# Performance work log

Hardware: AMD Instinct MI355X
Metric: run time of the kernel (lower is better)

The kernel has to match this reference:

```python
import jax, jax.numpy as jnp
import numpy as np

B, C, T = 64, 128, 4096
KNOT = 4  # default knot=4 -> 6 spline knots
SIGMA = 0.2


def setup_inputs() -> dict:
    key = jax.random.key(0)
    k1, k2, k3 = jax.random.split(key, 3)
    x = jax.random.normal(k1, (B, C, T), dtype=jnp.float32)
    # yy ~ N(1.0, sigma) as in GenerateRandomCurves
    yy = 1.0 + SIGMA * jax.random.normal(k2, (B, KNOT + 2, C), dtype=jnp.float32)
    mask_rand = jax.random.uniform(k3, (B, 1, 1), dtype=jnp.float32)
    return {"x": x, "yy": yy, "mask_rand": mask_rand}


def _notaknot_matrix(n, h):
    # Moment (second-derivative) system for a not-a-knot cubic spline on a
    # uniform grid with spacing h (matches scipy.interpolate.CubicSpline default bc).
    A = np.zeros((n, n), dtype=np.float32)
    for i in range(1, n - 1):
        A[i, i - 1] = h / 6.0
        A[i, i] = 2.0 * h / 3.0
        A[i, i + 1] = h / 6.0
    # not-a-knot: third derivative continuous at x1 and x_{n-2}
    A[0, 0], A[0, 1], A[0, 2] = 1.0, -2.0, 1.0
    A[-1, -3], A[-1, -2], A[-1, -1] = 1.0, -2.0, 1.0
    return jnp.asarray(A)


def reference(x, yy, mask_rand):
    Bq, Cq, Tq = x.shape
    n = KNOT + 2
    h = (Tq - 1) / (KNOT + 1)  # uniform knot spacing; knots span [0, T-1]
    A = _notaknot_matrix(n, h)

    # Solve for spline moments M (second derivatives at knots), batched over (B, C).
    rhs_int = (yy[:, 2:, :] - 2.0 * yy[:, 1:-1, :] + yy[:, :-2, :]) / h  # (B, n-2, C)
    z = jnp.zeros((Bq, 1, Cq), yy.dtype)
    rhs = jnp.concatenate([z, rhs_int, z], axis=1)  # (B, n, C)
    M = jnp.linalg.solve(A, rhs)  # (B, n, C)

    # Evaluate the spline at t = 0..T-1 (vectorized over all batch/channel).
    tq = jnp.arange(Tq, dtype=x.dtype)
    idx = jnp.clip(jnp.floor(tq / h).astype(jnp.int32), 0, n - 2)  # (T,)
    xl = idx.astype(x.dtype) * h
    dxl = (tq - xl)[None, :, None]       # t - x_i
    dxr = (xl + h - tq)[None, :, None]   # x_{i+1} - t
    Mi, Mi1 = M[:, idx, :], M[:, idx + 1, :]      # (B, T, C)
    yi, yi1 = yy[:, idx, :], yy[:, idx + 1, :]    # (B, T, C)
    curve = ((Mi * dxr**3 + Mi1 * dxl**3) / (6.0 * h)
             + (yi / h - Mi * h / 6.0) * dxr
             + (yi1 / h - Mi1 * h / 6.0) * dxl)   # (B, T, C)

    # DistortTimesteps: cumulative sum, rescaled so the last step lands on T-1.
    tt = jnp.cumsum(curve, axis=1)
    tt = tt * (Tq - 1) / tt[:, -1:, :]  # (B, T, C)

    # Per-(batch, channel) linear interpolation back onto the regular grid.
    xp = tt.transpose(0, 2, 1).reshape(Bq * Cq, Tq)  # warped timestamps
    fp = x.reshape(Bq * Cq, Tq)                      # channel signals
    x_tw = jax.vmap(lambda a, b: jnp.interp(tq, a, b))(xp, fp)
    x_tw = x_tw.reshape(Bq, Cq, Tq)

    mask = mask_rand < 0.5  # (B,1,1): apply warp with probability p=0.5
    return jnp.where(mask, x_tw, x)
```

## Files before the change

kernel.cpp:

```cpp
#include <hip/hip_runtime.h>

#define BB 64
#define CC 128
#define TT 4096
#define NN 6
#define HH 819.0f
#define NTHR 256
#define EPT 16
#define NWAVE (NTHR / 64)
#define NROW (BB * CC)
#define NSPAN 5
#define TABBYTES ((size_t)NROW * NSPAN * 16)
#define PADSZ (TT + TT / 32)

typedef float f4 __attribute__((ext_vector_type(4)));

__device__ __forceinline__ void nt_store4(float* p, f4 v) {
    __builtin_nontemporal_store(v, (f4*)p);
}

__device__ __forceinline__ int padi(int j) { return j + (j >> 5); }

__device__ __forceinline__ void spline_solve(const float* __restrict__ yy,
                                             int b, int c, float* y, float* Mv)
{
    #pragma unroll
    for (int k = 0; k < NN; ++k)
        y[k] = yy[((size_t)b * NN + k) * CC + c];
    float Aug[NN][NN + 1];
    #pragma unroll
    for (int i = 0; i < NN; ++i)
        #pragma unroll
        for (int j = 0; j < NN + 1; ++j)
            Aug[i][j] = 0.0f;
    Aug[0][0] = 1.0f;  Aug[0][1] = -2.0f;  Aug[0][2] = 1.0f;
    Aug[5][3] = 1.0f;  Aug[5][4] = -2.0f;  Aug[5][5] = 1.0f;
    #pragma unroll
    for (int i = 1; i < NN - 1; ++i) {
        Aug[i][i - 1] = HH / 6.0f;
        Aug[i][i]     = 2.0f * HH / 3.0f;
        Aug[i][i + 1] = HH / 6.0f;
        Aug[i][NN]    = (y[i + 1] - 2.0f * y[i] + y[i - 1]) / HH;
    }
    #pragma unroll
    for (int k = 0; k < NN; ++k) {
        float inv = 1.0f / Aug[k][k];
        #pragma unroll
        for (int i = k + 1; i < NN; ++i) {
            float m = Aug[i][k] * inv;
            #pragma unroll
            for (int j = k; j < NN + 1; ++j)
                Aug[i][j] -= m * Aug[k][j];
        }
    }
    #pragma unroll
    for (int i = NN - 1; i >= 0; --i) {
        float s = Aug[i][NN];
        #pragma unroll
        for (int j = i + 1; j < NN; ++j)
            s -= Aug[i][j] * Mv[j];
        Mv[i] = s / Aug[i][i];
    }
}

__device__ __forceinline__ void horner_coefs(const float* y, const float* Mv,
                                             f4* out5)
{
    const float invh  = 1.0f / HH;
    const float inv6h = 1.0f / (6.0f * HH);
    #pragma unroll
    for (int s = 0; s < NSPAN; ++s) {
        f4 cf;
        cf.x = y[s];
        cf.y = (y[s + 1] - y[s]) * invh - Mv[s] * (HH / 3.0f) - Mv[s + 1] * (HH / 6.0f);
        cf.z = Mv[s] * 0.5f;
        cf.w = (Mv[s + 1] - Mv[s]) * inv6h;
        out5[s] = cf;
    }
}

__global__ __launch_bounds__(256) void spline_coef_kernel(
    const float* __restrict__ yy, f4* __restrict__ tab)
{
    const int row = blockIdx.x * 256 + threadIdx.x;
    const int b = row / CC;
    const int c = row % CC;
    float y[NN], Mv[NN];
    spline_solve(yy, b, c, y, Mv);
    f4 cf[NSPAN];
    horner_coefs(y, Mv, cf);
    #pragma unroll
    for (int s = 0; s < NSPAN; ++s)
        tab[row * NSPAN + s] = cf[s];
}

template <int TABLE>
__global__ __launch_bounds__(NTHR, 6) void timewarp_kernel(
    const float* __restrict__ x,
    const float* __restrict__ yy,
    const float* __restrict__ mask_rand,
    const f4* __restrict__ tab,
    float* __restrict__ out)
{
    const int row = blockIdx.x;
    const int b   = row / CC;
    const int tid = threadIdx.x;

    const float* xrow = x + (size_t)row * TT;
    float* orow       = out + (size_t)row * TT;

    if (!(mask_rand[b] < 0.5f)) {
        const f4* xi = (const f4*)xrow;
        #pragma unroll
        for (int k = 0; k < 4; ++k)
            nt_store4(orow + 4 * (tid + NTHR * k), xi[tid + NTHR * k]);
        return;
    }

    __shared__ float sh_res[PADSZ];
    __shared__ float sh_wsum[NWAVE];

    const int t0 = tid * EPT;
    int idxA = t0 / 819;  if (idxA > 4) idxA = 4;
    int idxB = idxA + 1;  if (idxB > 4) idxB = 4;
    const float xlA = (float)idxA * HH;
    const float xlB = (float)idxB * HH;
    const float tb  = (float)((idxA + 1) * 819);

    float fpv[EPT];
    {
        #pragma unroll
        for (int q = 0; q < 4; ++q) {
            const f4 v = *(const f4*)(xrow + t0 + 4 * q);
            fpv[4 * q + 0] = v.x; fpv[4 * q + 1] = v.y;
            fpv[4 * q + 2] = v.z; fpv[4 * q + 3] = v.w;
        }
    }
    const float fpb = xrow[(t0 + EPT < TT) ? (t0 + EPT) : (TT - 1)];

    f4 cfA, cfB;
    if (TABLE) {
        cfA = tab[row * NSPAN + idxA];
        cfB = tab[row * NSPAN + idxB];
    } else {
        float y[NN], Mv[NN];
        f4 cf[NSPAN];
        spline_solve(yy, b, row % CC, y, Mv);
        horner_coefs(y, Mv, cf);
        cfA = cf[0];  cfB = cf[0];
        #pragma unroll
        for (int s = 1; s < NSPAN; ++s) {
            if (idxA >= s) cfA = cf[s];
            if (idxB >= s) cfB = cf[s];
        }
    }

    float xp[EPT + 1];
    float running = 0.0f;
    #pragma unroll
    for (int k = 0; k < EPT; ++k) {
        float ft = (float)(t0 + k);
        bool inB = ft >= tb;
        f4    cf = inB ? cfB : cfA;
        float xl = inB ? xlB : xlA;
        float s  = ft - xl;
        running += fmaf(s, fmaf(s, fmaf(s, cf.w, cf.z), cf.y), cf.x);
        xp[k] = running;
    }
    float cN;
    {
        float ft = (float)(t0 + EPT);
        bool inB = ft >= tb;
        f4    cf = inB ? cfB : cfA;
        float xl = inB ? xlB : xlA;
        float s  = ft - xl;
        cN = fmaf(s, fmaf(s, fmaf(s, cf.w, cf.z), cf.y), cf.x);
    }

    const int lane = tid & 63, wid = tid >> 6;
    float ws = running;
    #pragma unroll
    for (int d = 1; d < 64; d <<= 1) {
        float v = __shfl_up(ws, d, 64);
        if (lane >= d) ws += v;
    }
    if (lane == 63) sh_wsum[wid] = ws;
    __syncthreads();
    float wo = 0.0f, total = 0.0f;
    #pragma unroll
    for (int w = 0; w < NWAVE; ++w) {
        float s = sh_wsum[w];
        total += s;
        if (w < wid) wo += s;
    }
    const float offs  = wo + (ws - running);
    const float scale = 4095.0f / total;

    #pragma unroll
    for (int k = 0; k < EPT; ++k)
        xp[k] = (xp[k] + offs) * scale;

    {
        float n = __shfl_down(xp[0], 1, 64);
        float l = ((wo + ws) + cN) * scale;
        xp[EPT] = (lane == 63) ? l : n;
    }

    #pragma unroll
    for (int k = 0; k < EPT; ++k) {
        const int seg = t0 + k;
        if (seg < TT - 1) {
            float xa = xp[k], xb = xp[k + 1];
            float fa = fpv[k];
            float fb = (k < EPT - 1) ? fpv[k + 1] : fpb;
            float d  = xb - xa;
            float slope = (d > 0.0f) ? (fb - fa) * __builtin_amdgcn_rcpf(d) : 0.0f;
            float a0 = fmaf(-xa, slope, fa);
            int qlo = (int)ceilf(xa);  if (qlo < 0) qlo = 0;
            int qhi = (int)ceilf(xb);  if (qhi > TT) qhi = TT;
            for (int q = qlo; q < qhi; ++q)
                sh_res[padi(q)] = fmaf((float)q, slope, a0);
        }
    }
    if (tid == 0) {
        int q1 = (int)ceilf(xp[0]);  if (q1 > TT) q1 = TT;
        for (int q = 0; q < q1; ++q) sh_res[padi(q)] = fpv[0];
    }
    if (tid == NTHR - 1) {
        int q0 = (int)ceilf(xp[EPT - 1]);  if (q0 < 0) q0 = 0;
        for (int q = q0; q < TT; ++q) sh_res[padi(q)] = fpv[EPT - 1];
    }
    __syncthreads();

    #pragma unroll
    for (int kk = 0; kk < 4; ++kk) {
        int i4  = tid + NTHR * kk;
        int fb4 = 4 * i4;
        int p   = padi(fb4);
        f4 v;
        v.x = sh_res[p + 0];
        v.y = sh_res[p + 1];
        v.z = sh_res[p + 2];
        v.w = sh_res[p + 3];
        nt_store4(orow + fb4, v);
    }
}

extern "C" void kernel_launch(void* const* d_in, const int* in_sizes, int n_in,
                              void* d_out, int out_size, void* d_ws, size_t ws_size,
                              hipStream_t stream) {
    const float* x    = (const float*)d_in[0];
    const float* yy   = (const float*)d_in[1];
    const float* mask = (const float*)d_in[2];
    float* out = (float*)d_out;

    if (d_ws != nullptr && ws_size >= TABBYTES) {
        f4* tab = (f4*)d_ws;
        spline_coef_kernel<<<dim3(NROW / 256), dim3(256), 0, stream>>>(yy, tab);
        timewarp_kernel<1><<<dim3(NROW), dim3(NTHR), 0, stream>>>(x, yy, mask, tab, out);
    } else {
        timewarp_kernel<0><<<dim3(NROW), dim3(NTHR), 0, stream>>>(x, yy, mask, nullptr, out);
    }
}
```

Measured before the change: 241.6 us.

## Replace scatter interpolation with seeded per-quad search over shared xp/fp pairs

Instead of each source segment scattering interpolated values into a shared result buffer, the kernel now stores (xp, fp) pairs in shared memory and writes a coarse seed index for every group of four output positions. Each thread then starts from its seed and walks forward to find the bracketing segment for its four outputs before interpolating. The goal is to cut the per-output scatter work and load imbalance from uneven warping. In exchange it doubles the shared footprint with float2 entries, adds data-dependent while loops, and lowers the launch-bounds occupancy hint from 6 to 4.

```diff
diff --git a/kernel.cpp b/kernel.cpp
--- a/kernel.cpp
+++ b/kernel.cpp
@@ -11,7 +11,8 @@
 #define NROW (BB * CC)
 #define NSPAN 5
 #define TABBYTES ((size_t)NROW * NSPAN * 16)
-#define PADSZ (TT + TT / 32)
+#define NSEED 1024
+#define XFSZ 4224
 
 typedef float f4 __attribute__((ext_vector_type(4)));
 
@@ -19,7 +20,7 @@
     __builtin_nontemporal_store(v, (f4*)p);
 }
 
-__device__ __forceinline__ int padi(int j) { return j + (j >> 5); }
+__device__ __forceinline__ int p2(int j) { return j + (j >> 5); }
 
 __device__ __forceinline__ void spline_solve(const float* __restrict__ yy,
                                              int b, int c, float* y, float* Mv)
@@ -95,7 +96,7 @@
 }
 
 template <int TABLE>
-__global__ __launch_bounds__(NTHR, 6) void timewarp_kernel(
+__global__ __launch_bounds__(NTHR, 4) void timewarp_kernel(
     const float* __restrict__ x,
     const float* __restrict__ yy,
     const float* __restrict__ mask_rand,
@@ -117,8 +118,9 @@
         return;
     }
 
-    __shared__ float sh_res[PADSZ];
-    __shared__ float sh_wsum[NWAVE];
+    __shared__ float2 sh_xf[XFSZ];
+    __shared__ short  sh_seed[NSEED];
+    __shared__ float  sh_wsum[NWAVE];
 
     const int t0 = tid * EPT;
     int idxA = t0 / 819;  if (idxA > 4) idxA = 4;
@@ -136,7 +138,6 @@
             fpv[4 * q + 2] = v.z; fpv[4 * q + 3] = v.w;
         }
     }
-    const float fpb = xrow[(t0 + EPT < TT) ? (t0 + EPT) : (TT - 1)];
 
     f4 cfA, cfB;
     if (TABLE) {
@@ -207,42 +208,59 @@
     }
 
     #pragma unroll
+    for (int k = 0; k < EPT; ++k)
+        sh_xf[p2(t0 + k)] = make_float2(xp[k], fpv[k]);
+
+    #pragma unroll
     for (int k = 0; k < EPT; ++k) {
         const int seg = t0 + k;
         if (seg < TT - 1) {
             float xa = xp[k], xb = xp[k + 1];
-            float fa = fpv[k];
-            float fb = (k < EPT - 1) ? fpv[k + 1] : fpb;
-            float d  = xb - xa;
-            float slope = (d > 0.0f) ? (fb - fa) * __builtin_amdgcn_rcpf(d) : 0.0f;
-            float a0 = fmaf(-xa, slope, fa);
-            int qlo = (int)ceilf(xa);  if (qlo < 0) qlo = 0;
-            int qhi = (int)ceilf(xb);  if (qhi > TT) qhi = TT;
-            for (int q = qlo; q < qhi; ++q)
-                sh_res[padi(q)] = fmaf((float)q, slope, a0);
+            int m = (int)ceilf(xa * 0.25f);  if (m < 0) m = 0;
+            for (; m < NSEED && 4.0f * (float)m < xb; ++m)
+                sh_seed[m] = (short)seg;
         }
     }
     if (tid == 0) {
-        int q1 = (int)ceilf(xp[0]);  if (q1 > TT) q1 = TT;
-        for (int q = 0; q < q1; ++q) sh_res[padi(q)] = fpv[0];
+        int mh = (int)ceilf(xp[0] * 0.25f);  if (mh > NSEED) mh = NSEED;
+        for (int m = 0; m < mh; ++m) sh_seed[m] = (short)-1;
     }
     if (tid == NTHR - 1) {
-        int q0 = (int)ceilf(xp[EPT - 1]);  if (q0 < 0) q0 = 0;
-        for (int q = q0; q < TT; ++q) sh_res[padi(q)] = fpv[EPT - 1];
+        int mt = (int)ceilf(xp[EPT - 1] * 0.25f);  if (mt < 0) mt = 0;
+        for (int m = mt; m < NSEED; ++m) sh_seed[m] = (short)(TT - 1);
     }
     __syncthreads();
 
     #pragma unroll
-    for (int kk = 0; kk < 4; ++kk) {
-        int i4  = tid + NTHR * kk;
-        int fb4 = 4 * i4;
-        int p   = padi(fb4);
-        f4 v;
-        v.x = sh_res[p + 0];
-        v.y = sh_res[p + 1];
-        v.z = sh_res[p + 2];
-        v.w = sh_res[p + 3];
-        nt_store4(orow + fb4, v);
+    for (int ch = 0; ch < 4; ++ch) {
+        const int q0 = 4 * (tid + NTHR * ch);
+        int j = sh_seed[q0 >> 2];
+        float2 cur = sh_xf[p2(j < 0 ? 0 : j)];
+        if (j < 0) cur.x = -3.0e38f;
+        int j1 = j + 1;  if (j1 > TT - 1) j1 = TT - 1;
+        float2 nxt = sh_xf[p2(j1)];
+        f4 res;
+        #pragma unroll
+        for (int e = 0; e < 4; ++e) {
+            const float fq = (float)(q0 + e);
+            while (j < TT - 1 && nxt.x <= fq) {
+                ++j;
+                cur = nxt;
+                if (j < TT - 1) nxt = sh_xf[p2(j + 1)];
+            }
+            float v;
+            if (j >= TT - 1) {
+                v = cur.y;
+            } else {
+                float ratio = (fq - cur.x) * __builtin_amdgcn_rcpf(nxt.x - cur.x);
+                v = fmaf(ratio, nxt.y - cur.y, cur.y);
+            }
+            if (e == 0) res.x = v;
+            else if (e == 1) res.y = v;
+            else if (e == 2) res.z = v;
+            else res.w = v;
+        }
+        nt_store4(orow + q0, res);
     }
 }
 
```

New measurement: 239.1 us. No clear change (-1.1%).

## Process each row with a single wavefront instead of a 256-thread block

Applied to the files above, without the earlier changes.

Each row is now handled by one 64-lane wavefront that covers four 1024-sample chunks per lane, in place of a 256-thread block of four waves. The cumulative sum becomes a per-chunk wave scan plus chained chunk totals, which removes the __syncthreads barriers and the cross-wave shared-memory reduction. The cost is more sequential work and more registers per lane (64 loaded floats held live), with less parallelism per row. The final read-back of shared memory relies on lgkmcnt waits within a single wave rather than a barrier.

```diff
diff --git a/kernel.cpp b/kernel.cpp
--- a/kernel.cpp
+++ b/kernel.cpp
@@ -5,13 +5,12 @@
 #define TT 4096
 #define NN 6
 #define HH 819.0f
-#define NTHR 256
-#define EPT 16
-#define NWAVE (NTHR / 64)
 #define NROW (BB * CC)
 #define NSPAN 5
 #define TABBYTES ((size_t)NROW * NSPAN * 16)
 #define PADSZ (TT + TT / 32)
+#define CHN 4
+#define CEPT 16
 
 typedef float f4 __attribute__((ext_vector_type(4)));
 
@@ -95,16 +94,16 @@
 }
 
 template <int TABLE>
-__global__ __launch_bounds__(NTHR, 6) void timewarp_kernel(
+__global__ __launch_bounds__(64) void timewarp_kernel(
     const float* __restrict__ x,
     const float* __restrict__ yy,
     const float* __restrict__ mask_rand,
     const f4* __restrict__ tab,
     float* __restrict__ out)
 {
-    const int row = blockIdx.x;
-    const int b   = row / CC;
-    const int tid = threadIdx.x;
+    const int row  = blockIdx.x;
+    const int b    = row / CC;
+    const int lane = threadIdx.x;
 
     const float* xrow = x + (size_t)row * TT;
     float* orow       = out + (size_t)row * TT;
@@ -112,136 +111,168 @@
     if (!(mask_rand[b] < 0.5f)) {
         const f4* xi = (const f4*)xrow;
         #pragma unroll
-        for (int k = 0; k < 4; ++k)
-            nt_store4(orow + 4 * (tid + NTHR * k), xi[tid + NTHR * k]);
+        for (int k = 0; k < 16; ++k)
+            nt_store4(orow + 4 * (lane + 64 * k), xi[lane + 64 * k]);
         return;
     }
 
-    __shared__ float sh_res[PADSZ];
-    __shared__ float sh_wsum[NWAVE];
-
-    const int t0 = tid * EPT;
-    int idxA = t0 / 819;  if (idxA > 4) idxA = 4;
-    int idxB = idxA + 1;  if (idxB > 4) idxB = 4;
-    const float xlA = (float)idxA * HH;
-    const float xlB = (float)idxB * HH;
-    const float tb  = (float)((idxA + 1) * 819);
-
-    float fpv[EPT];
-    {
-        #pragma unroll
-        for (int q = 0; q < 4; ++q) {
-            const f4 v = *(const f4*)(xrow + t0 + 4 * q);
-            fpv[4 * q + 0] = v.x; fpv[4 * q + 1] = v.y;
-            fpv[4 * q + 2] = v.z; fpv[4 * q + 3] = v.w;
-        }
-    }
-    const float fpb = xrow[(t0 + EPT < TT) ? (t0 + EPT) : (TT - 1)];
-
-    f4 cfA, cfB;
+    __shared__ float sres[PADSZ];
+
+    int   idxA[CHN], idxB[CHN];
+    float xlA[CHN], xlB[CHN], tbb[CHN];
+    #pragma unroll
+    for (int c = 0; c < CHN; ++c) {
+        int t0c = c * 1024 + lane * CEPT;
+        int ia = t0c / 819;  if (ia > 4) ia = 4;
+        int ib = ia + 1;     if (ib > 4) ib = 4;
+        idxA[c] = ia;  idxB[c] = ib;
+        xlA[c] = (float)ia * HH;
+        xlB[c] = (float)ib * HH;
+        tbb[c] = (float)((ia + 1) * 819);
+    }
+
+    f4 fv[CHN * 4];
+    #pragma unroll
+    for (int c = 0; c < CHN; ++c)
+        #pragma unroll
+        for (int q = 0; q < 4; ++q)
+            fv[c * 4 + q] = *(const f4*)(xrow + c * 1024 + lane * CEPT + 4 * q);
+
+    f4 cfA[CHN], cfB[CHN];
     if (TABLE) {
-        cfA = tab[row * NSPAN + idxA];
-        cfB = tab[row * NSPAN + idxB];
+        #pragma unroll
+        for (int c = 0; c < CHN; ++c) {
+            cfA[c] = tab[row * NSPAN + idxA[c]];
+            cfB[c] = tab[row * NSPAN + idxB[c]];
+        }
     } else {
         float y[NN], Mv[NN];
         f4 cf[NSPAN];
         spline_solve(yy, b, row % CC, y, Mv);
         horner_coefs(y, Mv, cf);
-        cfA = cf[0];  cfB = cf[0];
-        #pragma unroll
-        for (int s = 1; s < NSPAN; ++s) {
-            if (idxA >= s) cfA = cf[s];
-            if (idxB >= s) cfB = cf[s];
-        }
-    }
-
-    float xp[EPT + 1];
-    float running = 0.0f;
-    #pragma unroll
-    for (int k = 0; k < EPT; ++k) {
-        float ft = (float)(t0 + k);
-        bool inB = ft >= tb;
-        f4    cf = inB ? cfB : cfA;
-        float xl = inB ? xlB : xlA;
-        float s  = ft - xl;
-        running += fmaf(s, fmaf(s, fmaf(s, cf.w, cf.z), cf.y), cf.x);
-        xp[k] = running;
-    }
-    float cN;
-    {
-        float ft = (float)(t0 + EPT);
-        bool inB = ft >= tb;
-        f4    cf = inB ? cfB : cfA;
-        float xl = inB ? xlB : xlA;
-        float s  = ft - xl;
-        cN = fmaf(s, fmaf(s, fmaf(s, cf.w, cf.z), cf.y), cf.x);
-    }
-
-    const int lane = tid & 63, wid = tid >> 6;
-    float ws = running;
-    #pragma unroll
-    for (int d = 1; d < 64; d <<= 1) {
-        float v = __shfl_up(ws, d, 64);
-        if (lane >= d) ws += v;
-    }
-    if (lane == 63) sh_wsum[wid] = ws;
-    __syncthreads();
-    float wo = 0.0f, total = 0.0f;
-    #pragma unroll
-    for (int w = 0; w < NWAVE; ++w) {
-        float s = sh_wsum[w];
-        total += s;
-        if (w < wid) wo += s;
-    }
-    const float offs  = wo + (ws - running);
-    const float scale = 4095.0f / total;
-
-    #pragma unroll
-    for (int k = 0; k < EPT; ++k)
-        xp[k] = (xp[k] + offs) * scale;
-
-    {
-        float n = __shfl_down(xp[0], 1, 64);
-        float l = ((wo + ws) + cN) * scale;
-        xp[EPT] = (lane == 63) ? l : n;
-    }
-
-    #pragma unroll
-    for (int k = 0; k < EPT; ++k) {
-        const int seg = t0 + k;
-        if (seg < TT - 1) {
-            float xa = xp[k], xb = xp[k + 1];
-            float fa = fpv[k];
-            float fb = (k < EPT - 1) ? fpv[k + 1] : fpb;
-            float d  = xb - xa;
-            float slope = (d > 0.0f) ? (fb - fa) * __builtin_amdgcn_rcpf(d) : 0.0f;
-            float a0 = fmaf(-xa, slope, fa);
-            int qlo = (int)ceilf(xa);  if (qlo < 0) qlo = 0;
-            int qhi = (int)ceilf(xb);  if (qhi > TT) qhi = TT;
-            for (int q = qlo; q < qhi; ++q)
-                sh_res[padi(q)] = fmaf((float)q, slope, a0);
-        }
-    }
-    if (tid == 0) {
-        int q1 = (int)ceilf(xp[0]);  if (q1 > TT) q1 = TT;
-        for (int q = 0; q < q1; ++q) sh_res[padi(q)] = fpv[0];
-    }
-    if (tid == NTHR - 1) {
-        int q0 = (int)ceilf(xp[EPT - 1]);  if (q0 < 0) q0 = 0;
-        for (int q = q0; q < TT; ++q) sh_res[padi(q)] = fpv[EPT - 1];
-    }
-    __syncthreads();
-
-    #pragma unroll
-    for (int kk = 0; kk < 4; ++kk) {
-        int i4  = tid + NTHR * kk;
+        #pragma unroll
+        for (int c = 0; c < CHN; ++c) {
+            f4 a = cf[0], bb = cf[0];
+            #pragma unroll
+            for (int s = 1; s < NSPAN; ++s) {
+                if (idxA[c] >= s) a  = cf[s];
+                if (idxB[c] >= s) bb = cf[s];
+            }
+            cfA[c] = a;  cfB[c] = bb;
+        }
+    }
+
+    float ct[CHN];
+    #pragma unroll
+    for (int c = 0; c < CHN; ++c) {
+        float t0f = (float)(c * 1024 + lane * CEPT);
+        float acc = 0.0f;
+        #pragma unroll
+        for (int k = 0; k < CEPT; ++k) {
+            float ft = t0f + (float)k;
+            bool inB = ft >= tbb[c];
+            f4    cf = inB ? cfB[c] : cfA[c];
+            float s  = ft - (inB ? xlB[c] : xlA[c]);
+            acc += fmaf(s, fmaf(s, fmaf(s, cf.w, cf.z), cf.y), cf.x);
+        }
+        ct[c] = acc;
+    }
+
+    float incl[CHN], excl[CHN], ctT[CHN];
+    #pragma unroll
+    for (int c = 0; c < CHN; ++c) {
+        float v = ct[c];
+        #pragma unroll
+        for (int d = 1; d < 64; d <<= 1) {
+            float u = __shfl_up(v, d, 64);
+            if (lane >= d) v += u;
+        }
+        incl[c] = v;
+        excl[c] = __shfl_up(v, 1, 64);
+        ctT[c]  = __shfl(v, 63, 64);
+    }
+    float cp[CHN + 1];
+    cp[0] = 0.0f;
+    #pragma unroll
+    for (int c = 0; c < CHN; ++c)
+        cp[c + 1] = cp[c] + ctT[c];
+    const float scale = 4095.0f / cp[CHN];
+
+    #pragma unroll
+    for (int c = 0; c < CHN; ++c) {
+        const int   t0i = c * 1024 + lane * CEPT;
+        const float t0f = (float)t0i;
+        float run = (lane == 0) ? cp[c] : (cp[c] + excl[c]);
+        float xp[CEPT + 1];
+        #pragma unroll
+        for (int k = 0; k < CEPT; ++k) {
+            float ft = t0f + (float)k;
+            bool inB = ft >= tbb[c];
+            f4    cf = inB ? cfB[c] : cfA[c];
+            float s  = ft - (inB ? xlB[c] : xlA[c]);
+            run += fmaf(s, fmaf(s, fmaf(s, cf.w, cf.z), cf.y), cf.x);
+            xp[k] = run * scale;
+        }
+        {
+            float ft = t0f + (float)CEPT;
+            bool inB = ft >= tbb[c];
+            f4    cf = inB ? cfB[c] : cfA[c];
+            float s  = ft - (inB ? xlB[c] : xlA[c]);
+            float cN = fmaf(s, fmaf(s, fmaf(s, cf.w, cf.z), cf.y), cf.x);
+            xp[CEPT] = ((cp[c] + incl[c]) + cN) * scale;
+        }
+
+        float fpl[CEPT];
+        #pragma unroll
+        for (int q = 0; q < 4; ++q) {
+            f4 v = fv[c * 4 + q];
+            fpl[4 * q + 0] = v.x; fpl[4 * q + 1] = v.y;
+            fpl[4 * q + 2] = v.z; fpl[4 * q + 3] = v.w;
+        }
+        float fb;
+        {
+            float nxt_same  = __shfl_down(fv[c * 4].x, 1, 64);
+            float nxt_chunk = __shfl(fv[((c + 1) & 3) * 4].x, 0, 64);
+            fb = (lane == 63) ? nxt_chunk : nxt_same;
+        }
+
+        #pragma unroll
+        for (int k = 0; k < CEPT; ++k) {
+            const int seg = t0i + k;
+            if (seg < TT - 1) {
+                float xa = xp[k], xb = xp[k + 1];
+                float fa = fpl[k];
+                float fbk = (k < CEPT - 1) ? fpl[k + 1] : fb;
+                float d  = xb - xa;
+                float slope = (d > 0.0f) ? (fbk - fa) * __builtin_amdgcn_rcpf(d) : 0.0f;
+                float a0 = fmaf(-xa, slope, fa);
+                int qlo = (int)ceilf(xa);  if (qlo < 0) qlo = 0;
+                int qhi = (int)ceilf(xb);  if (qhi > TT) qhi = TT;
+                for (int q = qlo; q < qhi; ++q)
+                    sres[padi(q)] = fmaf((float)q, slope, a0);
+            }
+        }
+        if (c == 0 && lane == 0) {
+            int q1 = (int)ceilf(xp[0]);  if (q1 > TT) q1 = TT;
+            for (int q = 0; q < q1; ++q) sres[padi(q)] = fpl[0];
+        }
+        if (c == CHN - 1 && lane == 63) {
+            int q0 = (int)ceilf(xp[CEPT - 1]);  if (q0 < 0) q0 = 0;
+            for (int q = q0; q < TT; ++q) sres[padi(q)] = fpl[CEPT - 1];
+        }
+    }
+
+    asm volatile("s_waitcnt lgkmcnt(0)" ::: "memory");
+    #pragma unroll
+    for (int k = 0; k < 16; ++k) {
+        int i4  = lane + 64 * k;
         int fb4 = 4 * i4;
         int p   = padi(fb4);
         f4 v;
-        v.x = sh_res[p + 0];
-        v.y = sh_res[p + 1];
-        v.z = sh_res[p + 2];
-        v.w = sh_res[p + 3];
+        v.x = sres[p + 0];
+        v.y = sres[p + 1];
+        v.z = sres[p + 2];
+        v.w = sres[p + 3];
         nt_store4(orow + fb4, v);
     }
 }
@@ -257,8 +288,8 @@
     if (d_ws != nullptr && ws_size >= TABBYTES) {
         f4* tab = (f4*)d_ws;
         spline_coef_kernel<<<dim3(NROW / 256), dim3(256), 0, stream>>>(yy, tab);
-        timewarp_kernel<1><<<dim3(NROW), dim3(NTHR), 0, stream>>>(x, yy, mask, tab, out);
+        timewarp_kernel<1><<<dim3(NROW), dim3(64), 0, stream>>>(x, yy, mask, tab, out);
     } else {
-        timewarp_kernel<0><<<dim3(NROW), dim3(NTHR), 0, stream>>>(x, yy, mask, nullptr, out);
-    }
-}
+        timewarp_kernel<0><<<dim3(NROW), dim3(64), 0, stream>>>(x, yy, mask, nullptr, out);
+    }
+}
```

Measured after the change: 262.2 us. 8.5% more time.
